# Optimization experiments

Measured on AMD Instinct MI355X. Metric: run time of the kernel, lower is better.

Reference implementation:

```python
import jax, jax.numpy as jnp
import numpy as np

MAX_LEN = 1024
DIM = 1024
NUM_HEADS = 16
DIM_HEAD = 64
BATCH = 8


def _pos_emb(max_len, dim):
    pos_seq = jnp.arange(max_len - 1, -1, -1.0, dtype=jnp.float32)
    inv_freq = 1.0 / (10000.0 ** (jnp.arange(0, dim, 2.0, dtype=jnp.float32) / dim))
    sinusoid = jnp.einsum('i,j->ij', pos_seq, inv_freq)
    return jnp.concatenate([jnp.sin(sinusoid), jnp.cos(sinusoid)], axis=-1)  # [S, dim]


def _rel_shift(x):
    # x: [B, H, I, J] -> Transformer-XL relative shift
    b, h, i, j = x.shape
    x = jnp.pad(x, ((0, 0), (0, 0), (0, 0), (1, 0)))
    x = x.reshape(b, h, j + 1, i)[:, :, 1:, :]
    return x.reshape(b, h, i, j)


def setup_inputs() -> dict:
    key = jax.random.key(0)
    k1, k2, k3, k4 = jax.random.split(key, 4)
    inputs = jax.random.normal(k1, (BATCH, MAX_LEN, DIM), dtype=jnp.float32)
    mask = jnp.ones((BATCH, MAX_LEN), dtype=bool)
    Wqkv = jax.random.normal(k2, (DIM, 3 * NUM_HEADS * DIM_HEAD), dtype=jnp.float32) * 0.02
    Wr = jax.random.normal(k3, (DIM, NUM_HEADS * DIM_HEAD), dtype=jnp.float32) * 0.02
    Wo = jax.random.normal(k4, (NUM_HEADS * DIM_HEAD, DIM), dtype=jnp.float32) * 0.02
    return {"inputs": inputs, "mask": mask, "Wqkv": Wqkv, "Wr": Wr, "Wo": Wo}


def reference(inputs, mask, Wqkv, Wr, Wo):
    B, S, dim = inputs.shape
    H, Dh = NUM_HEADS, DIM_HEAD
    scale = 1.0 / (Dh ** 0.5)

    qkv = jnp.einsum('bsd,de->bse', inputs, Wqkv)  # [B,S,3*H*Dh]
    q, k, v = jnp.split(qkv, 3, axis=-1)
    q = q.reshape(B, S, H, Dh)
    k = k.reshape(B, S, H, Dh)
    v = v.reshape(B, S, H, Dh)

    pos = _pos_emb(S, dim)                          # [S, dim]
    r = jnp.einsum('sd,de->se', pos, Wr).reshape(S, H, Dh)  # [S,H,Dh]

    AC = jnp.einsum('bihd,bjhd->bhij', q, k)        # content score
    BD = jnp.einsum('bihd,jhd->bhij', q, r)         # position score
    BD = _rel_shift(BD)
    score = (AC + BD) * scale

    att_mask = mask[:, None, None, :].astype(score.dtype)
    score = score * att_mask - 1e30 * (1.0 - att_mask)

    prob = jax.nn.softmax(score, axis=-1)
    attn_vec = jnp.einsum('bhij,bjhd->bihd', prob, v).reshape(B, S, H * Dh)
    out = jnp.einsum('bse,ed->bsd', attn_vec, Wo)
    return out + inputs
```

## Files before the change

### kernel.cpp

```cpp
#include <hip/hip_runtime.h>

#define SQL 1024
#define NHD 16
#define DHD 64
#define NB  8

typedef unsigned short u16;
typedef short s16x8 __attribute__((ext_vector_type(8)));
typedef __bf16 b16x8 __attribute__((ext_vector_type(8)));
typedef float f32x4 __attribute__((ext_vector_type(4)));
typedef u16 u16x4 __attribute__((ext_vector_type(4)));
typedef u16 u16x8 __attribute__((ext_vector_type(8)));
typedef unsigned int u32x4 __attribute__((ext_vector_type(4)));

static __device__ __forceinline__ u16 f2b(float f) {
  unsigned u = __float_as_uint(f);
  u += 0x7fffu + ((u >> 16) & 1u);
  return (u16)(u >> 16);
}
static __device__ __forceinline__ float b2f(u16 v) {
  return __uint_as_float(((unsigned)v) << 16);
}

template <typename V>
static __device__ __forceinline__ auto mfma_sel(V a, V b, f32x4 c, int)
    -> decltype(__builtin_amdgcn_mfma_f32_16x16x32_bf16(a, b, c, 0, 0, 0)) {
  return __builtin_amdgcn_mfma_f32_16x16x32_bf16(a, b, c, 0, 0, 0);
}
template <typename V>
static __device__ __forceinline__ f32x4 mfma_sel(V a, V b, f32x4 c, long) {
  return __builtin_amdgcn_mfma_f32_16x16x32_bf16(
      __builtin_bit_cast(b16x8, a), __builtin_bit_cast(b16x8, b), c, 0, 0, 0);
}
static __device__ __forceinline__ f32x4 MFMA(s16x8 a, s16x8 b, f32x4 c) {
  return mfma_sel(a, b, c, 0);
}

static __device__ __forceinline__ void gload16(const u16* g, u16* l) {
  __builtin_amdgcn_global_load_lds(
      (const __attribute__((address_space(1))) unsigned int*)g,
      (__attribute__((address_space(3))) unsigned int*)l, 16, 0, 0);
}

__global__ __launch_bounds__(256) void cvt_kernel(const float* __restrict__ src,
                                                  u16* __restrict__ dst, int n4) {
  int idx = blockIdx.x * 256 + threadIdx.x;
  if (idx < n4) {
    f32x4 v = reinterpret_cast<const f32x4*>(src)[idx];
    u16x4 o;
    o[0] = f2b(v[0]); o[1] = f2b(v[1]); o[2] = f2b(v[2]); o[3] = f2b(v[3]);
    reinterpret_cast<u16x4*>(dst)[idx] = o;
  }
}

__global__ __launch_bounds__(256) void transpose_cvt(const float* __restrict__ src,
                                                     u16* __restrict__ dst,
                                                     int R, int C) {
  __shared__ float tile[32][33];
  int bx = blockIdx.x * 32;
  int by = blockIdx.y * 32;
  int tx = threadIdx.x & 31, ty = threadIdx.x >> 5;
  #pragma unroll
  for (int r = ty; r < 32; r += 8)
    tile[r][tx] = src[(size_t)(by + r) * C + bx + tx];
  __syncthreads();
  #pragma unroll
  for (int r = ty; r < 32; r += 8)
    dst[(size_t)(bx + r) * R + by + tx] = f2b(tile[tx][r]);
}

__global__ __launch_bounds__(256) void pos_kernel(u16* __restrict__ posb) {
  int idx = blockIdx.x * 256 + threadIdx.x;
  int s = idx >> 10, j = idx & 1023;
  int t = (j < 512) ? j : j - 512;
  float freq = __expf(-(float)(2 * t) * (logf(10000.f) / 1024.f));
  float ang = (float)(1023 - s) * freq;
  posb[idx] = f2b((j < 512) ? sinf(ang) : cosf(ang));
}

__global__ __launch_bounds__(256) void vt_kernel(const u16* __restrict__ qkv,
                                                 u16* __restrict__ vT) {
  int bh = blockIdx.x;
  int b = bh >> 4, h = bh & 15;
  int j0 = blockIdx.y * 64;
  __shared__ __align__(16) u16 tile[64][72];
  int tid = threadIdx.x;
  for (int idx = tid; idx < 512; idx += 256) {
    int j = idx >> 3, c = (idx & 7) * 8;
    *reinterpret_cast<u32x4*>(&tile[j][c]) = *reinterpret_cast<const u32x4*>(
        &qkv[(size_t)(b * SQL + j0 + j) * 3072 + 2048 + h * 64 + c]);
  }
  __syncthreads();
  for (int idx = tid; idx < 512; idx += 256) {
    int d = idx >> 3, c = (idx & 7) * 8;
    u16x8 pk;
    #pragma unroll
    for (int e = 0; e < 8; ++e) pk[e] = tile[c + e][d];
    *reinterpret_cast<u16x8*>(
        &vT[(size_t)bh * DHD * SQL + (size_t)d * SQL + j0 + c]) = pk;
  }
}

template <int OUT>
__global__ __launch_bounds__(256) void gemm97(
    const u16* __restrict__ A, const u16* __restrict__ Bt, void* __restrict__ Cv,
    const float* __restrict__ resid, int K, int lda, int ldb, int ldc,
    int bandH) {
  __shared__ __align__(16) u16 at[128 * 64];
  __shared__ __align__(16) u16 bt[128 * 64];

  int bid = blockIdx.x;
  int xcd = bid & 7, loc = bid >> 3;
  int m0 = (xcd * bandH + (loc % bandH)) * 128;
  int n0 = (loc / bandH) * 128;

  const int tid = threadIdx.x, lane = tid & 63, w = tid >> 6;
  const int wm = (w & 1) * 64, wn = (w >> 1) * 64;
  const int fr = lane & 15, kg = lane >> 4;
  const int lrow = lane >> 3, lcol = (lane & 7) * 8;

  f32x4 acc[4][4] = {};

  for (int k0 = 0; k0 < K; k0 += 64) {
    __syncthreads();
    #pragma unroll
    for (int ci = 0; ci < 4; ++ci) {
      int ch = w * 4 + ci;
      gload16(&A[(size_t)(m0 + ch * 8 + lrow) * lda + k0 + lcol], &at[ch * 512]);
      gload16(&Bt[(size_t)(n0 + ch * 8 + lrow) * ldb + k0 + lcol], &bt[ch * 512]);
    }
    __syncthreads();

    #pragma unroll
    for (int ks = 0; ks < 2; ++ks) {
      s16x8 af[4], bf[4];
      #pragma unroll
      for (int i = 0; i < 4; ++i) {
        af[i] = *(const s16x8*)&at[(wm + i * 16 + fr) * 64 + ks * 32 + kg * 8];
        bf[i] = *(const s16x8*)&bt[(wn + i * 16 + fr) * 64 + ks * 32 + kg * 8];
      }
      #pragma unroll
      for (int mi = 0; mi < 4; ++mi)
        #pragma unroll
        for (int ni = 0; ni < 4; ++ni)
          acc[mi][ni] = MFMA(af[mi], bf[ni], acc[mi][ni]);
    }
  }

  #pragma unroll
  for (int mi = 0; mi < 4; ++mi)
    #pragma unroll
    for (int ni = 0; ni < 4; ++ni)
      #pragma unroll
      for (int rr = 0; rr < 4; ++rr) {
        int rrow = m0 + wm + mi * 16 + kg * 4 + rr;
        int ccol = n0 + wn + ni * 16 + fr;
        size_t ci = (size_t)rrow * ldc + ccol;
        float v = acc[mi][ni][rr];
        if constexpr (OUT == 1) ((u16*)Cv)[ci] = f2b(v);
        else ((float*)Cv)[ci] = v + resid[ci];
      }
}

template <int BM, int BN, int WM, int WN>
__global__ __launch_bounds__(WM * WN * 64) void bdgemm_kernel(
    const u16* __restrict__ A, const u16* __restrict__ Bt, u16* __restrict__ Cv,
    int lda, int ldb, int zbase) {
  constexpr int NT = WM * WN * 64;
  constexpr int FM = BM / WM / 16;
  constexpr int FN = BN / WN / 16;
  __shared__ __align__(16) u16 at[BM][40];
  __shared__ __align__(16) u16 bt[BN][40];

  int zg = zbase + blockIdx.z;
  int bb = zg >> 4, hh = zg & 15;
  A += (size_t)bb * SQL * 3072 + (size_t)hh * 64;
  Bt += (size_t)hh * 64;
  u16* bd = Cv + (size_t)blockIdx.z * SQL * SQL;

  const int tid = threadIdx.x;
  const int lane = tid & 63;
  const int w = tid >> 6;
  const int wm = (w / WN) * (FM * 16);
  const int wn = (w % WN) * (FN * 16);
  const int m0 = blockIdx.x * BM;
  const int n0 = blockIdx.y * BN;
  const int fr = lane & 15;
  const int kb = (lane >> 4) * 8;

  f32x4 acc[FM][FN] = {};

  for (int k0 = 0; k0 < 64; k0 += 32) {
    __syncthreads();
    for (int idx = tid; idx < BM * 4; idx += NT) {
      int r = idx >> 2, c = (idx & 3) << 3;
      *reinterpret_cast<u32x4*>(&at[r][c]) = *reinterpret_cast<const u32x4*>(
          &A[(size_t)(m0 + r) * lda + k0 + c]);
    }
    for (int idx = tid; idx < BN * 4; idx += NT) {
      int r = idx >> 2, c = (idx & 3) << 3;
      *reinterpret_cast<u32x4*>(&bt[r][c]) = *reinterpret_cast<const u32x4*>(
          &Bt[(size_t)(n0 + r) * ldb + k0 + c]);
    }
    __syncthreads();

    s16x8 af[FM], bfr[FN];
    #pragma unroll
    for (int mi = 0; mi < FM; ++mi)
      af[mi] = *reinterpret_cast<const s16x8*>(&at[wm + mi * 16 + fr][kb]);
    #pragma unroll
    for (int ni = 0; ni < FN; ++ni)
      bfr[ni] = *reinterpret_cast<const s16x8*>(&bt[wn + ni * 16 + fr][kb]);
    #pragma unroll
    for (int mi = 0; mi < FM; ++mi)
      #pragma unroll
      for (int ni = 0; ni < FN; ++ni)
        acc[mi][ni] = MFMA(af[mi], bfr[ni], acc[mi][ni]);
  }

  const int orow = (lane >> 4) << 2;
  const int ocol = lane & 15;
  #pragma unroll
  for (int mi = 0; mi < FM; ++mi)
    #pragma unroll
    for (int ni = 0; ni < FN; ++ni)
      #pragma unroll
      for (int rr = 0; rr < 4; ++rr) {
        int rrow = m0 + wm + mi * 16 + orow + rr;
        int ccol = n0 + wn + ni * 16 + ocol;
        u16 bv = f2b(acc[mi][ni][rr]);
        int j1 = rrow + ccol - (SQL - 1);
        if (j1 >= 0) bd[(size_t)rrow * SQL + j1] = bv;
        int j2 = rrow + ccol + 1;
        if (rrow >= 1 && j2 < SQL) bd[(size_t)(rrow - 1) * SQL + j2] = bv;
      }
  if (n0 == 0 && tid < BM) {
    int i = m0 + tid;
    if (i + 1 < SQL) bd[(size_t)i * SQL + i + 1] = 0;
  }
}

#define TLD 72
#define SC2 0.180336880f
#define THR2 11.5416f

__global__ __launch_bounds__(256, 4) void attn_kernel(
    const u16* __restrict__ qkv, const u16* __restrict__ cb,
    const u16* __restrict__ vT, u16* __restrict__ att, int zbase, int CH) {
  __shared__ __align__(16) u16 kl[64 * TLD];
  __shared__ __align__(16) u16 vl[64 * TLD];
  __shared__ __align__(16) u16 pl[64 * TLD];
  __shared__ __align__(16) u16 bdl[64 * TLD];

  int bid = blockIdx.x;
  int z, qt;
  if ((CH * 16) % 8 == 0) {
    int per = CH * 2;
    int swz = (bid & 7) * per + (bid >> 3);
    z = swz >> 4; qt = swz & 15;
  } else {
    z = bid >> 4; qt = bid & 15;
  }
  int bh = zbase + z;
  int b = bh >> 4, h = bh & 15;
  int i0 = qt * 64;

  const int tid = threadIdx.x, lane = tid & 63, w = tid >> 6;
  const int fr = lane & 15, kg = lane >> 4, kb8 = kg * 8;
  const int srow = tid >> 3, sc8 = (tid & 7) * 8;
  const int myrow = w * 16 + fr;

  s16x8 aq[2];
  {
    const u16* qp = &qkv[(size_t)(b * SQL + i0 + myrow) * 3072 + h * 64 + kb8];
    aq[0] = *(const s16x8*)qp;
    aq[1] = *(const s16x8*)(qp + 32);
  }

  const u16* kbase = &qkv[(size_t)(b * SQL) * 3072 + 1024 + h * 64];
  const u16* vbase = &vT[(size_t)bh * 64 * 1024];
  const u16* bdbase = &cb[(size_t)z * SQL * SQL + (size_t)i0 * SQL];

  u32x4 kA0, kA1, vA0, vA1, bA0, bA1;
  u32x4 kB0, kB1, vB0, vB1, bB0, bB1;

  auto ISSUE = [&](u32x4& K0, u32x4& K1, u32x4& V0, u32x4& V1, u32x4& B0,
                   u32x4& B1, int t) {
    int j0 = t * 64;
    K0 = *(const u32x4*)&kbase[(size_t)(j0 + srow) * 3072 + sc8];
    K1 = *(const u32x4*)&kbase[(size_t)(j0 + srow + 32) * 3072 + sc8];
    V0 = *(const u32x4*)&vbase[(size_t)srow * 1024 + j0 + sc8];
    V1 = *(const u32x4*)&vbase[(size_t)(srow + 32) * 1024 + j0 + sc8];
    B0 = *(const u32x4*)&bdbase[(size_t)srow * SQL + j0 + sc8];
    B1 = *(const u32x4*)&bdbase[(size_t)(srow + 32) * SQL + j0 + sc8];
  };
  auto COMMIT = [&](u32x4 K0, u32x4 K1, u32x4 V0, u32x4 V1, u32x4 B0,
                    u32x4 B1) {
    *(u32x4*)&kl[srow * TLD + sc8] = K0;
    *(u32x4*)&kl[(srow + 32) * TLD + sc8] = K1;
    *(u32x4*)&vl[srow * TLD + sc8] = V0;
    *(u32x4*)&vl[(srow + 32) * TLD + sc8] = V1;
    *(u32x4*)&bdl[srow * TLD + sc8] = B0;
    *(u32x4*)&bdl[(srow + 32) * TLD + sc8] = B1;
  };

  f32x4 acco[4] = {};
  float mreg = -1e30f, lreg = 0.f;

  auto BODY = [&](int j0) {
    f32x4 st[4] = {};
    #pragma unroll
    for (int nf = 0; nf < 4; ++nf)
      #pragma unroll
      for (int ks = 0; ks < 2; ++ks)
        st[nf] = MFMA(*(const s16x8*)&kl[(nf * 16 + fr) * TLD + ks * 32 + kb8],
                      aq[ks], st[nf]);

    float s0[4][4];
    float rmax = -1e30f;
    #pragma unroll
    for (int nf = 0; nf < 4; ++nf) {
      u16x4 bdv = *(const u16x4*)&bdl[myrow * TLD + nf * 16 + kg * 4];
      #pragma unroll
      for (int rr = 0; rr < 4; ++rr) {
        s0[nf][rr] = (st[nf][rr] + b2f(bdv[rr])) * SC2;
        rmax = fmaxf(rmax, s0[nf][rr]);
      }
    }
    rmax = fmaxf(rmax, __shfl_xor(rmax, 16));
    rmax = fmaxf(rmax, __shfl_xor(rmax, 32));
    if (rmax > mreg + THR2) {
      float sf = exp2f(mreg - rmax);
      mreg = rmax;
      lreg *= sf;
      #pragma unroll
      for (int mf = 0; mf < 4; ++mf) acco[mf] *= sf;
    }
    float ps = 0.f;
    #pragma unroll
    for (int nf = 0; nf < 4; ++nf) {
      u16x4 pp;
      #pragma unroll
      for (int rr = 0; rr < 4; ++rr) {
        float p = exp2f(s0[nf][rr] - mreg);
        ps += p;
        pp[rr] = f2b(p);
      }
      *(u16x4*)&pl[myrow * TLD + nf * 16 + kg * 4] = pp;
    }
    ps += __shfl_xor(ps, 16);
    ps += __shfl_xor(ps, 32);
    lreg += ps;

    s16x8 ap0 = *(const s16x8*)&pl[myrow * TLD + kb8];
    s16x8 ap1 = *(const s16x8*)&pl[myrow * TLD + 32 + kb8];
    #pragma unroll
    for (int mf = 0; mf < 4; ++mf) {
      acco[mf] = MFMA(*(const s16x8*)&vl[(mf * 16 + fr) * TLD + kb8], ap0,
                      acco[mf]);
      acco[mf] = MFMA(*(const s16x8*)&vl[(mf * 16 + fr) * TLD + 32 + kb8], ap1,
                      acco[mf]);
    }
  };

  ISSUE(kA0, kA1, vA0, vA1, bA0, bA1, 0);
  for (int tt = 0; tt < 16; tt += 2) {
    __syncthreads();
    COMMIT(kA0, kA1, vA0, vA1, bA0, bA1);
    __syncthreads();
    ISSUE(kB0, kB1, vB0, vB1, bB0, bB1, tt + 1);
    BODY(tt * 64);

    __syncthreads();
    COMMIT(kB0, kB1, vB0, vB1, bB0, bB1);
    __syncthreads();
    if (tt < 14) ISSUE(kA0, kA1, vA0, vA1, bA0, bA1, tt + 2);
    BODY((tt + 1) * 64);
  }

  {
    float inv = 1.0f / lreg;
    size_t base = (size_t)(b * SQL + i0 + myrow) * 1024 + h * 64;
    #pragma unroll
    for (int mf = 0; mf < 4; ++mf) {
      u16x4 o;
      #pragma unroll
      for (int rr = 0; rr < 4; ++rr) o[rr] = f2b(acco[mf][rr] * inv);
      *(u16x4*)&att[base + mf * 16 + kg * 4] = o;
    }
  }
}

extern "C" void kernel_launch(void* const* d_in, const int* in_sizes, int n_in,
                              void* d_out, int out_size, void* d_ws, size_t ws_size,
                              hipStream_t stream) {
  const float* inputs = (const float*)d_in[0];
  const float* Wqkv = (const float*)d_in[2];
  const float* Wr = (const float*)d_in[3];
  const float* Wo = (const float*)d_in[4];
  float* out = (float*)d_out;

  char* ws = (char*)d_ws;
  size_t off = 0;
  auto alloc = [&](size_t bytes) -> char* {
    char* p = ws + off;
    off = (off + bytes + 255) & ~(size_t)255;
    return p;
  };
  u16* Xb    = (u16*)alloc(8192ULL * 1024 * 2);
  u16* WqkvT = (u16*)alloc(3072ULL * 1024 * 2);
  u16* WrT   = (u16*)alloc(1024ULL * 1024 * 2);
  u16* WoT   = (u16*)alloc(1024ULL * 1024 * 2);
  u16* posb  = (u16*)alloc(1024ULL * 1024 * 2);
  u16* rb    = (u16*)alloc(1024ULL * 1024 * 2);
  u16* qkvb  = (u16*)alloc(8192ULL * 3072 * 2);
  u16* vT    = (u16*)alloc(128ULL * 64 * 1024 * 2);
  u16* att   = (u16*)alloc(8192ULL * 1024 * 2);
  size_t fixedBytes = off;

  int CH = 8;
  const int cands[5] = {128, 64, 32, 16, 8};
  for (int t = 0; t < 5; ++t) {
    size_t need = fixedBytes + (size_t)cands[t] * SQL * SQL * 2 + 1024;
    if (need <= ws_size) { CH = cands[t]; break; }
  }
  u16* cbuf = (u16*)alloc((size_t)CH * SQL * SQL * 2);

  cvt_kernel<<<dim3(8192), dim3(256), 0, stream>>>(inputs, Xb, 8192 * 1024 / 4);
  transpose_cvt<<<dim3(96, 32), dim3(256), 0, stream>>>(Wqkv, WqkvT, 1024, 3072);
  transpose_cvt<<<dim3(32, 32), dim3(256), 0, stream>>>(Wr, WrT, 1024, 1024);
  transpose_cvt<<<dim3(32, 32), dim3(256), 0, stream>>>(Wo, WoT, 1024, 1024);
  pos_kernel<<<dim3(4096), dim3(256), 0, stream>>>(posb);

  gemm97<1><<<dim3(64), dim3(256), 0, stream>>>(
      posb, WrT, rb, nullptr, 1024, 1024, 1024, 1024, 1);
  gemm97<1><<<dim3(1536), dim3(256), 0, stream>>>(
      Xb, WqkvT, qkvb, nullptr, 1024, 1024, 1024, 3072, 8);
  vt_kernel<<<dim3(128, 16), dim3(256), 0, stream>>>(qkvb, vT);

  for (int z0 = 0; z0 < NB * NHD; z0 += CH) {
    bdgemm_kernel<128, 128, 2, 2><<<dim3(8, 8, CH), dim3(256), 0, stream>>>(
        qkvb, rb, cbuf, 3072, 1024, z0);
    attn_kernel<<<dim3(CH * 16), dim3(256), 0, stream>>>(
        qkvb, cbuf, vT, att, z0, CH);
  }

  gemm97<2><<<dim3(512), dim3(256), 0, stream>>>(
      att, WoT, out, inputs, 1024, 1024, 1024, 1024, 8);
}
```

Baseline: 380.2 us.

## Alias temp buffers with score chunk buffer and retile output projection GEMM

Workspace layout is reorganized so the bf16 input, transposed Wqkv/Wr and positional buffers share storage with the BD score chunk buffer, since they are dead after the early GEMMs. This lets the per-chunk count be chosen from the remaining space, capped at 32 instead of 128, and changes how many bdgemm/attn launch pairs run. The GEMM is templated on tile shape, and the output projection uses 128x64 tiles with twice as many blocks for better CU occupancy. The lower chunk cap may add launches, and the aliasing depends on correct stream ordering.

```diff
diff --git a/kernel.cpp b/kernel.cpp
--- a/kernel.cpp
+++ b/kernel.cpp
@@ -101,56 +101,62 @@
   }
 }
 
-template <int OUT>
+template <int BM, int BN, int OUT>
 __global__ __launch_bounds__(256) void gemm97(
     const u16* __restrict__ A, const u16* __restrict__ Bt, void* __restrict__ Cv,
     const float* __restrict__ resid, int K, int lda, int ldb, int ldc,
     int bandH) {
-  __shared__ __align__(16) u16 at[128 * 64];
-  __shared__ __align__(16) u16 bt[128 * 64];
+  constexpr int FM = BM / 32, FN = BN / 32;
+  __shared__ __align__(16) u16 at[BM * 64];
+  __shared__ __align__(16) u16 bt[BN * 64];
 
   int bid = blockIdx.x;
   int xcd = bid & 7, loc = bid >> 3;
-  int m0 = (xcd * bandH + (loc % bandH)) * 128;
-  int n0 = (loc / bandH) * 128;
+  int m0 = (xcd * bandH + (loc % bandH)) * BM;
+  int n0 = (loc / bandH) * BN;
 
   const int tid = threadIdx.x, lane = tid & 63, w = tid >> 6;
-  const int wm = (w & 1) * 64, wn = (w >> 1) * 64;
+  const int wm = (w & 1) * (BM / 2), wn = (w >> 1) * (BN / 2);
   const int fr = lane & 15, kg = lane >> 4;
   const int lrow = lane >> 3, lcol = (lane & 7) * 8;
 
-  f32x4 acc[4][4] = {};
+  f32x4 acc[FM][FN] = {};
 
   for (int k0 = 0; k0 < K; k0 += 64) {
     __syncthreads();
     #pragma unroll
-    for (int ci = 0; ci < 4; ++ci) {
-      int ch = w * 4 + ci;
+    for (int ci = 0; ci < FM; ++ci) {
+      int ch = w * FM + ci;
       gload16(&A[(size_t)(m0 + ch * 8 + lrow) * lda + k0 + lcol], &at[ch * 512]);
+    }
+    #pragma unroll
+    for (int ci = 0; ci < FN; ++ci) {
+      int ch = w * FN + ci;
       gload16(&Bt[(size_t)(n0 + ch * 8 + lrow) * ldb + k0 + lcol], &bt[ch * 512]);
     }
     __syncthreads();
 
     #pragma unroll
     for (int ks = 0; ks < 2; ++ks) {
-      s16x8 af[4], bf[4];
-      #pragma unroll
-      for (int i = 0; i < 4; ++i) {
+      s16x8 af[FM], bf[FN];
+      #pragma unroll
+      for (int i = 0; i < FM; ++i)
         af[i] = *(const s16x8*)&at[(wm + i * 16 + fr) * 64 + ks * 32 + kg * 8];
+      #pragma unroll
+      for (int i = 0; i < FN; ++i)
         bf[i] = *(const s16x8*)&bt[(wn + i * 16 + fr) * 64 + ks * 32 + kg * 8];
-      }
-      #pragma unroll
-      for (int mi = 0; mi < 4; ++mi)
+      #pragma unroll
+      for (int mi = 0; mi < FM; ++mi)
         #pragma unroll
-        for (int ni = 0; ni < 4; ++ni)
+        for (int ni = 0; ni < FN; ++ni)
           acc[mi][ni] = MFMA(af[mi], bf[ni], acc[mi][ni]);
     }
   }
 
   #pragma unroll
-  for (int mi = 0; mi < 4; ++mi)
-    #pragma unroll
-    for (int ni = 0; ni < 4; ++ni)
+  for (int mi = 0; mi < FM; ++mi)
+    #pragma unroll
+    for (int ni = 0; ni < FN; ++ni)
       #pragma unroll
       for (int rr = 0; rr < 4; ++rr) {
         int rrow = m0 + wm + mi * 16 + kg * 4 + rr;
@@ -407,24 +413,25 @@
     off = (off + bytes + 255) & ~(size_t)255;
     return p;
   };
-  u16* Xb    = (u16*)alloc(8192ULL * 1024 * 2);
-  u16* WqkvT = (u16*)alloc(3072ULL * 1024 * 2);
-  u16* WrT   = (u16*)alloc(1024ULL * 1024 * 2);
-  u16* WoT   = (u16*)alloc(1024ULL * 1024 * 2);
-  u16* posb  = (u16*)alloc(1024ULL * 1024 * 2);
-  u16* rb    = (u16*)alloc(1024ULL * 1024 * 2);
-  u16* qkvb  = (u16*)alloc(8192ULL * 3072 * 2);
-  u16* vT    = (u16*)alloc(128ULL * 64 * 1024 * 2);
-  u16* att   = (u16*)alloc(8192ULL * 1024 * 2);
-  size_t fixedBytes = off;
-
-  int CH = 8;
-  const int cands[5] = {128, 64, 32, 16, 8};
-  for (int t = 0; t < 5; ++t) {
-    size_t need = fixedBytes + (size_t)cands[t] * SQL * SQL * 2 + 1024;
-    if (need <= ws_size) { CH = cands[t]; break; }
-  }
-  u16* cbuf = (u16*)alloc((size_t)CH * SQL * SQL * 2);
+  u16* qkvb = (u16*)alloc(8192ULL * 3072 * 2);
+  u16* vT   = (u16*)alloc(128ULL * 64 * 1024 * 2);
+  u16* att  = (u16*)alloc(8192ULL * 1024 * 2);
+  u16* rb   = (u16*)alloc(1024ULL * 1024 * 2);
+  u16* WoT  = (u16*)alloc(1024ULL * 1024 * 2);
+
+  size_t remain = (ws_size > off) ? (ws_size - off) : 0;
+  char* tbase = ws + off;
+  u16* Xb    = (u16*)tbase;
+  u16* WqkvT = (u16*)(tbase + 16777216);
+  u16* WrT   = (u16*)(tbase + 16777216 + 6291456);
+  u16* posb  = (u16*)(tbase + 16777216 + 6291456 + 2097152);
+  u16* cbuf  = (u16*)tbase;
+
+  int CH = 1;
+  const int cands[6] = {32, 16, 8, 4, 2, 1};
+  for (int t = 0; t < 6; ++t) {
+    if ((size_t)cands[t] * SQL * SQL * 2 + 1024 <= remain) { CH = cands[t]; break; }
+  }
 
   cvt_kernel<<<dim3(8192), dim3(256), 0, stream>>>(inputs, Xb, 8192 * 1024 / 4);
   transpose_cvt<<<dim3(96, 32), dim3(256), 0, stream>>>(Wqkv, WqkvT, 1024, 3072);
@@ -432,9 +439,9 @@
   transpose_cvt<<<dim3(32, 32), dim3(256), 0, stream>>>(Wo, WoT, 1024, 1024);
   pos_kernel<<<dim3(4096), dim3(256), 0, stream>>>(posb);
 
-  gemm97<1><<<dim3(64), dim3(256), 0, stream>>>(
+  gemm97<128, 128, 1><<<dim3(64), dim3(256), 0, stream>>>(
       posb, WrT, rb, nullptr, 1024, 1024, 1024, 1024, 1);
-  gemm97<1><<<dim3(1536), dim3(256), 0, stream>>>(
+  gemm97<128, 128, 1><<<dim3(1536), dim3(256), 0, stream>>>(
       Xb, WqkvT, qkvb, nullptr, 1024, 1024, 1024, 3072, 8);
   vt_kernel<<<dim3(128, 16), dim3(256), 0, stream>>>(qkvb, vT);
 
@@ -445,6 +452,6 @@
         qkvb, cbuf, vT, att, z0, CH);
   }
 
-  gemm97<2><<<dim3(512), dim3(256), 0, stream>>>(
+  gemm97<128, 64, 2><<<dim3(1024), dim3(256), 0, stream>>>(
       att, WoT, out, inputs, 1024, 1024, 1024, 1024, 8);
 }
```

Measured after the change: 418.3 us. +10.0%, slower.
